# Kernel optimization log

Hardware: AMD Instinct MI355X
Metric: run time of the kernel (lower is better)

The kernel has to match this reference:

```python
import math
import jax, jax.numpy as jnp
import numpy as np

T = 2048       # sequence_length
H = 2048       # hidden_size
NH = 32        # num_attention_heads
NKV = 8        # num_key_value_heads
HD = 64        # head_dim
SW = 128       # sliding_window
QM = NH // NKV # q_mult (GQA group size)
ROPE_THETA = 10000.0
EPS = 1e-5


def setup_inputs() -> dict:
    key = jax.random.key(0)
    k_x, k_s, k_qkv, k_out = jax.random.split(key, 4)
    x = jax.random.normal(k_x, (T, H), dtype=jnp.float32)
    scale = jnp.ones((H,), dtype=jnp.float32)
    sinks = jax.random.normal(k_s, (NH,), dtype=jnp.float32) * 0.02
    qkv_dim = HD * (NH + 2 * NKV)  # 3072
    qkv_kernel = jax.random.normal(k_qkv, (H, qkv_dim), dtype=jnp.float32) * (1.0 / math.sqrt(H))
    qkv_bias = jnp.zeros((qkv_dim,), dtype=jnp.float32)
    out_kernel = jax.random.normal(k_out, (H, H), dtype=jnp.float32) * (1.0 / math.sqrt(H))
    out_bias = jnp.zeros((H,), dtype=jnp.float32)
    # RoPE tables: [T, HD//2]
    half = HD // 2
    inv_freq = 1.0 / (ROPE_THETA ** (np.arange(half, dtype=np.float64) / half))
    ang = np.outer(np.arange(T, dtype=np.float64), inv_freq)
    cos_table = jnp.asarray(np.cos(ang), dtype=jnp.float32)
    sin_table = jnp.asarray(np.sin(ang), dtype=jnp.float32)
    # causal + sliding-window additive mask [T, T]
    qp = np.arange(T, dtype=np.int32)[:, None]
    kp = np.arange(T, dtype=np.int32)[None, :]
    m = np.where(kp > qp, -np.inf, 0.0) + np.where(qp - kp > SW, -np.inf, 0.0)
    mask = jnp.asarray(m, dtype=jnp.float32)
    return dict(x=x, scale=scale, sinks=sinks, qkv_kernel=qkv_kernel,
                qkv_bias=qkv_bias, out_kernel=out_kernel, out_bias=out_bias,
                cos_table=cos_table, sin_table=sin_table, mask=mask)


def _rmsnorm(x, scale):
    t = x.astype(jnp.float32)
    rms = jnp.sqrt(jnp.mean(t * t, axis=-1, keepdims=True) + EPS)
    return ((t / rms) * scale).astype(x.dtype)


def _rope(x, cos, sin):
    # x: [T, ..., HD]; split-half rotation as in the reference RotaryEmbedding
    shp = x.shape
    xr = x.reshape(shp[0], -1, HD)
    c = cos[:, None, :].astype(xr.dtype)
    s = sin[:, None, :].astype(xr.dtype)
    x1, x2 = jnp.split(xr, 2, axis=-1)
    y = jnp.concatenate([x1 * c - x2 * s, x2 * c + x1 * s], axis=-1)
    return y.reshape(shp)


def reference(x, scale, sinks, qkv_kernel, qkv_bias, out_kernel, out_bias,
              cos_table, sin_table, mask):
    normed = _rmsnorm(x, scale)
    qkv = normed @ qkv_kernel + qkv_bias                 # [T, 3072]
    q_end = NH * HD
    k_end = q_end + NKV * HD
    q = qkv[:, :q_end].reshape(T, NKV, QM, HD)           # [T, nkv, qm, hd]
    k = qkv[:, q_end:k_end].reshape(T, NKV, HD)          # [T, nkv, hd]
    v = qkv[:, k_end:].reshape(T, NKV, HD)               # [T, nkv, hd]
    q = _rope(q, cos_table, sin_table)
    k = _rope(k, cos_table, sin_table)
    sm_scale = 1.0 / math.sqrt(float(HD))
    # GQA attention without materializing repeated K/V
    logits = jnp.einsum('qnmd,knd->nmqk', q, k) * sm_scale  # [nkv, qm, T, T]
    logits = logits + mask[None, None, :, :]
    sink_col = jnp.broadcast_to(sinks.reshape(NKV, QM, 1, 1), (NKV, QM, T, 1))
    logits = jnp.concatenate([logits, sink_col], axis=-1)   # [nkv, qm, T, T+1]
    weights = jax.nn.softmax(logits, axis=-1)[..., :-1]     # drop sink column
    attn = jnp.einsum('nmqk,knd->qnmd', weights, v).reshape(T, NH * HD)
    projected = attn @ out_kernel + out_bias
    return x + projected
```

## Files before the change

kernel.cpp:

```cpp
#include <hip/hip_runtime.h>
#include <hip/hip_bf16.h>
#include <stdint.h>

typedef __bf16 bf16_t;
typedef __attribute__((ext_vector_type(8))) __bf16 bf16x8;
typedef __attribute__((ext_vector_type(4))) __bf16 bf16x4;
typedef __attribute__((ext_vector_type(4))) float f32x4;

static constexpr int T_SEQ = 2048;
static constexpr int HID   = 2048;
static constexpr int NHEAD = 32;
static constexpr int NKVH  = 8;
static constexpr int HDIM  = 64;
static constexpr int QKVD  = 3072;

__device__ inline f32x4 mfma16(bf16x8 a, bf16x8 b, f32x4 c) {
    return __builtin_amdgcn_mfma_f32_16x16x32_bf16(a, b, c, 0, 0, 0);
}

__device__ inline void load_lds16(const bf16_t* g, bf16_t* l) {
    __builtin_amdgcn_global_load_lds(
        (const __attribute__((address_space(1))) void*)g,
        (__attribute__((address_space(3))) void*)l, 16, 0, 0);
}

__global__ __launch_bounds__(256) void prep_kernel(const float* __restrict__ Wq,
                                                   const float* __restrict__ Wo,
                                                   bf16_t* __restrict__ Tq,
                                                   bf16_t* __restrict__ To,
                                                   const float* __restrict__ x,
                                                   const float* __restrict__ scale,
                                                   bf16_t* __restrict__ normed) {
    __shared__ float tile[64 * 65];
    int b = blockIdx.x;
    const int t = threadIdx.x;
    if (b < 2560) {
        const float* in; bf16_t* outw; int NN, KK, bx, by;
        if (b < 1536) { in = Wq; outw = Tq; NN = QKVD; KK = HID; bx = b % 48; by = b / 48; }
        else { b -= 1536; in = Wo; outw = To; NN = HID; KK = HID; bx = b % 32; by = b / 32; }
        const int c4 = (t & 15) * 4;
#pragma unroll
        for (int i = 0; i < 4; ++i) {
            int r = (t >> 4) + i * 16;
            float4 v = *(const float4*)(in + (size_t)(by*64 + r) * NN + bx*64 + c4);
            tile[r*65 + c4 + 0] = v.x; tile[r*65 + c4 + 1] = v.y;
            tile[r*65 + c4 + 2] = v.z; tile[r*65 + c4 + 3] = v.w;
        }
        __syncthreads();
        const int kc = t & 7;
#pragma unroll
        for (int i = 0; i < 2; ++i) {
            int n = (t >> 3) + i * 32;
            bf16x8 o;
#pragma unroll
            for (int j = 0; j < 8; ++j) o[j] = (bf16_t)tile[(kc*8 + j)*65 + n];
            *(bf16x8*)(outw + (size_t)(bx*64 + n) * KK + by*64 + kc*8) = o;
        }
    } else {
        int row = b - 2560;
        const float4* x4 = (const float4*)(x + (size_t)row * HID);
        const float4* s4 = (const float4*)scale;
        float4 v0 = x4[t], v1 = x4[t + 256];
        float ss = v0.x*v0.x + v0.y*v0.y + v0.z*v0.z + v0.w*v0.w
                 + v1.x*v1.x + v1.y*v1.y + v1.z*v1.z + v1.w*v1.w;
#pragma unroll
        for (int off = 32; off > 0; off >>= 1) ss += __shfl_down(ss, off);
        if ((t & 63) == 0) tile[t >> 6] = ss;
        __syncthreads();
        float total = tile[0] + tile[1] + tile[2] + tile[3];
        float inv = rsqrtf(total * (1.0f / HID) + 1e-5f);
        float4 sc0 = s4[t], sc1 = s4[t + 256];
        bf16_t* outr = normed + (size_t)row * HID;
        bf16x4 o0, o1;
        o0.x = (bf16_t)(v0.x*inv*sc0.x); o0.y = (bf16_t)(v0.y*inv*sc0.y);
        o0.z = (bf16_t)(v0.z*inv*sc0.z); o0.w = (bf16_t)(v0.w*inv*sc0.w);
        o1.x = (bf16_t)(v1.x*inv*sc1.x); o1.y = (bf16_t)(v1.y*inv*sc1.y);
        o1.z = (bf16_t)(v1.z*inv*sc1.z); o1.w = (bf16_t)(v1.w*inv*sc1.w);
        *(bf16x4*)(outr + 4*t)        = o0;
        *(bf16x4*)(outr + 1024 + 4*t) = o1;
    }
}

__global__ __launch_bounds__(256) void gemm_splitk(const bf16_t* __restrict__ A,
                                                   const bf16_t* __restrict__ Bt,
                                                   bf16_t* __restrict__ Cpart,
                                                   int M, int N, int K) {
    __shared__ __align__(16) bf16_t Asm[3 * 128 * 32];
    __shared__ __align__(16) bf16_t Bsm[3 * 128 * 32];
    const int tid = threadIdx.x;
    const int bm = blockIdx.y * 128, bn = blockIdx.x * 128;
    const int kh = K >> 1;
    const int kb = blockIdx.z * kh;
    const int lane = tid & 63, wave = tid >> 6;
    const int wm = (wave & 1) * 64, wn = (wave >> 1) * 64;
    const int lm = lane & 15, quad = lane >> 4;

    f32x4 acc[4][4];
#pragma unroll
    for (int i = 0; i < 4; ++i)
#pragma unroll
        for (int j = 0; j < 4; ++j) acc[i][j] = (f32x4){0.f, 0.f, 0.f, 0.f};

    const int cid0 = tid, cid1 = tid + 256;
    const int r0 = cid0 >> 2, c0 = (cid0 & 3) ^ ((r0 >> 1) & 3);
    const int r1 = cid1 >> 2, c1 = (cid1 & 3) ^ ((r1 >> 1) & 3);
    const bf16_t* Ab = A  + (size_t)bm * K + kb;
    const bf16_t* Bb = Bt + (size_t)bn * K + kb;
    const size_t ga0 = (size_t)r0 * K + c0 * 8;
    const size_t ga1 = (size_t)r1 * K + c1 * 8;
    const int swz = (quad ^ ((lm >> 1) & 3)) * 8;
    const int ldso = wave * 512;

    const int nsteps = kh >> 5;

#define STAGE(buf, k0) do {                               \
        bf16_t* la_ = &Asm[(buf) * 4096];                 \
        bf16_t* lb_ = &Bsm[(buf) * 4096];                 \
        load_lds16(Ab + ga0 + (k0), la_ + ldso);          \
        load_lds16(Ab + ga1 + (k0), la_ + 2048 + ldso);   \
        load_lds16(Bb + ga0 + (k0), lb_ + ldso);          \
        load_lds16(Bb + ga1 + (k0), lb_ + 2048 + ldso);   \
    } while (0)

    STAGE(0, 0);
    STAGE(1, 32);

    int cur = 0, nxt = 2;
    for (int t = 0; t < nsteps; ++t) {
        if (t + 1 < nsteps) asm volatile("s_waitcnt vmcnt(4)" ::: "memory");
        else                asm volatile("s_waitcnt vmcnt(0)" ::: "memory");
        __builtin_amdgcn_s_barrier();
        __builtin_amdgcn_sched_barrier(0);
        if (t + 2 < nsteps) STAGE(nxt, (t + 2) * 32);

        const bf16_t* __restrict__ Abase = &Asm[cur * 4096];
        const bf16_t* __restrict__ Bbase = &Bsm[cur * 4096];
        bf16x8 af[4], bfr[4];
#pragma unroll
        for (int i = 0; i < 4; ++i)
            af[i]  = *(const bf16x8*)&Abase[(wm + i*16 + lm)*32 + swz];
#pragma unroll
        for (int j = 0; j < 4; ++j)
            bfr[j] = *(const bf16x8*)&Bbase[(wn + j*16 + lm)*32 + swz];
#pragma unroll
        for (int i = 0; i < 4; ++i)
#pragma unroll
            for (int j = 0; j < 4; ++j) acc[i][j] = mfma16(af[i], bfr[j], acc[i][j]);

        cur = (cur == 2) ? 0 : cur + 1;
        nxt = (nxt == 2) ? 0 : nxt + 1;
    }
#undef STAGE

    bf16_t* Cp = Cpart + (size_t)blockIdx.z * M * N;
#pragma unroll
    for (int i = 0; i < 4; ++i) {
        int gr = bm + wm + i*16 + quad*4;
#pragma unroll
        for (int j = 0; j < 4; ++j) {
            int gc = bn + wn + j*16 + lm;
#pragma unroll
            for (int r = 0; r < 4; ++r)
                Cp[(size_t)(gr + r)*N + gc] = (bf16_t)acc[i][j][r];
        }
    }
}

__global__ __launch_bounds__(192) void rope_split(const bf16_t* __restrict__ qp0,
                                                  const bf16_t* __restrict__ qp1,
                                                  const float* __restrict__ qbias,
                                                  const float* __restrict__ cost,
                                                  const float* __restrict__ sint,
                                                  bf16_t* __restrict__ Qb,
                                                  bf16_t* __restrict__ Kb,
                                                  bf16_t* __restrict__ Vb) {
    const int t = blockIdx.x;
    const int hr = threadIdx.x >> 2, p0 = (threadIdx.x & 3) * 8;
    const bf16_t* r0 = qp0 + (size_t)t * QKVD + hr * 64;
    const bf16_t* r1 = qp1 + (size_t)t * QKVD + hr * 64;
    bf16x8 a1 = *(const bf16x8*)(r0 + p0);
    bf16x8 a2 = *(const bf16x8*)(r0 + p0 + 32);
    bf16x8 b1 = *(const bf16x8*)(r1 + p0);
    bf16x8 b2 = *(const bf16x8*)(r1 + p0 + 32);
    const float* qb = qbias + hr * 64;
    float x1[8], x2[8];
#pragma unroll
    for (int j = 0; j < 8; ++j) {
        x1[j] = (float)a1[j] + (float)b1[j] + qb[p0 + j];
        x2[j] = (float)a2[j] + (float)b2[j] + qb[p0 + j + 32];
    }
    bf16x8 w1, w2;
    if (hr < 40) {
        const float* c = cost + (size_t)t * 32 + p0;
        const float* s = sint + (size_t)t * 32 + p0;
#pragma unroll
        for (int j = 0; j < 8; ++j) {
            float cc = c[j], ss = s[j];
            w1[j] = (bf16_t)(x1[j]*cc - x2[j]*ss);
            w2[j] = (bf16_t)(x2[j]*cc + x1[j]*ss);
        }
    } else {
#pragma unroll
        for (int j = 0; j < 8; ++j) { w1[j] = (bf16_t)x1[j]; w2[j] = (bf16_t)x2[j]; }
    }
    bf16_t* dst;
    if (hr < 32)      dst = Qb + ((size_t)t*NHEAD + hr)      * HDIM;
    else if (hr < 40) dst = Kb + ((size_t)t*NKVH + (hr-32))  * HDIM;
    else              dst = Vb + ((size_t)t*NKVH + (hr-40))  * HDIM;
    *(bf16x8*)(dst + p0)      = w1;
    *(bf16x8*)(dst + p0 + 32) = w2;
}

__global__ __launch_bounds__(256) void combine_out(const bf16_t* __restrict__ p0,
                                                   const bf16_t* __restrict__ p1,
                                                   const float* __restrict__ bias,
                                                   const float* __restrict__ x,
                                                   float* __restrict__ out) {
    const int n4 = T_SEQ * HID / 4;
    for (int i4 = blockIdx.x * 256 + threadIdx.x; i4 < n4; i4 += gridDim.x * 256) {
        bf16x4 a = *(const bf16x4*)(p0 + (size_t)i4 * 4);
        bf16x4 b = *(const bf16x4*)(p1 + (size_t)i4 * 4);
        float4 xv = *(const float4*)(x + (size_t)i4 * 4);
        int col4 = (i4 * 4) & (HID - 1);
        float4 bi = *(const float4*)(bias + col4);
        float4 o;
        o.x = (float)a.x + (float)b.x + bi.x + xv.x;
        o.y = (float)a.y + (float)b.y + bi.y + xv.y;
        o.z = (float)a.z + (float)b.z + bi.z + xv.z;
        o.w = (float)a.w + (float)b.w + bi.w + xv.w;
        *(float4*)(out + (size_t)i4 * 4) = o;
    }
}

__global__ __launch_bounds__(256) void attn_kernel(const bf16_t* __restrict__ Qb,
                                                   const bf16_t* __restrict__ Kb,
                                                   const bf16_t* __restrict__ Vb,
                                                   const float* __restrict__ sinks,
                                                   bf16_t* __restrict__ attnb) {
    __shared__ __align__(16) bf16_t Vt[64 * 200];
    __shared__ __align__(16) bf16_t Ws[64 * 200];

    const int tid = threadIdx.x;
    const int qt = blockIdx.x, h = blockIdx.y;
    const int qs = qt * 64;
    const int nkv = h >> 2;

    {
        const int off = (tid >> 5) * 8;
#pragma unroll
        for (int it = 0; it < 3; ++it) {
            int j2 = (tid & 31) + 32 * it;
            int kg0 = qs - 128 + 2*j2;     if (kg0 < 0) kg0 = 0;
            int kg1 = qs - 128 + 2*j2 + 1; if (kg1 < 0) kg1 = 0;
            union { uint4 u; bf16_t e[8]; } v0, v1;
            v0.u = *(const uint4*)(Vb + ((size_t)kg0*NKVH + nkv)*HDIM + off);
            v1.u = *(const uint4*)(Vb + ((size_t)kg1*NKVH + nkv)*HDIM + off);
#pragma unroll
            for (int r = 0; r < 8; ++r) {
                union { uint u; bf16_t e[2]; } p;
                p.e[0] = v0.e[r]; p.e[1] = v1.e[r];
                *(uint*)&Vt[(off + r)*200 + 2*j2] = p.u;
            }
        }
    }

    const int lane = tid & 63, wave = tid >> 6;
    const int lm = lane & 15, quad = lane >> 4;
    const int w16 = wave * 16;

    f32x4 S[12];
#pragma unroll
    for (int jt = 0; jt < 12; ++jt) S[jt] = (f32x4){0.f, 0.f, 0.f, 0.f};
    const bf16_t* Qrow = Qb + ((size_t)(qs + w16 + lm)*NHEAD + h)*HDIM + quad*8;
    int krow[12];
#pragma unroll
    for (int jt = 0; jt < 12; ++jt) {
        int kg = qs - 128 + jt*16 + lm;
        krow[jt] = kg < 0 ? 0 : kg;
    }
#pragma unroll
    for (int ks = 0; ks < 2; ++ks) {
        bf16x8 aq = *(const bf16x8*)(Qrow + ks*32);
#pragma unroll
        for (int jt = 0; jt < 12; ++jt) {
            bf16x8 bk = *(const bf16x8*)(Kb + ((size_t)krow[jt]*NKVH + nkv)*HDIM + ks*32 + quad*8);
            S[jt] = mfma16(aq, bk, S[jt]);
        }
    }

    const float sink = sinks[h];
#pragma unroll
    for (int reg = 0; reg < 4; ++reg) {
        const int qg = qs + w16 + quad*4 + reg;
        float mx = -1e30f;
#pragma unroll
        for (int jt = 0; jt < 12; ++jt) {
            int kg = qs - 128 + jt*16 + lm;
            float sv = S[jt][reg] * 0.125f;
            bool valid = (kg >= 0) && (kg <= qg) && (qg - kg <= 128);
            sv = valid ? sv : -1e30f;
            S[jt][reg] = sv;
            mx = fmaxf(mx, sv);
        }
#pragma unroll
        for (int off = 1; off < 16; off <<= 1) mx = fmaxf(mx, __shfl_xor(mx, off));
        float M = fmaxf(mx, sink);
        float sum = 0.f;
#pragma unroll
        for (int jt = 0; jt < 12; ++jt) {
            float e = __expf(S[jt][reg] - M);
            S[jt][reg] = e; sum += e;
        }
#pragma unroll
        for (int off = 1; off < 16; off <<= 1) sum += __shfl_xor(sum, off);
        float rden = 1.f / (sum + __expf(sink - M));
#pragma unroll
        for (int jt = 0; jt < 12; ++jt)
            Ws[(w16 + quad*4 + reg)*200 + jt*16 + lm] = (bf16_t)(S[jt][reg] * rden);
    }
    __syncthreads();

    f32x4 O[4];
#pragma unroll
    for (int nt = 0; nt < 4; ++nt) O[nt] = (f32x4){0.f, 0.f, 0.f, 0.f};
#pragma unroll
    for (int ks = 0; ks < 6; ++ks) {
        bf16x8 aw = *(const bf16x8*)&Ws[(w16 + lm)*200 + ks*32 + quad*8];
#pragma unroll
        for (int nt = 0; nt < 4; ++nt) {
            bf16x8 bv = *(const bf16x8*)&Vt[(nt*16 + lm)*200 + ks*32 + quad*8];
            O[nt] = mfma16(aw, bv, O[nt]);
        }
    }
#pragma unroll
    for (int nt = 0; nt < 4; ++nt)
#pragma unroll
        for (int reg = 0; reg < 4; ++reg)
            attnb[(size_t)(qs + w16 + quad*4 + reg)*HID + h*HDIM + nt*16 + lm] =
                (bf16_t)(O[nt][reg]);
}

extern "C" void kernel_launch(void* const* d_in, const int* in_sizes, int n_in,
                              void* d_out, int out_size, void* d_ws, size_t ws_size,
                              hipStream_t stream) {
    (void)in_sizes; (void)n_in; (void)out_size; (void)ws_size;
    const float* x          = (const float*)d_in[0];
    const float* scale      = (const float*)d_in[1];
    const float* sinks      = (const float*)d_in[2];
    const float* qkv_kernel = (const float*)d_in[3];
    const float* qkv_bias   = (const float*)d_in[4];
    const float* out_kernel = (const float*)d_in[5];
    const float* out_bias   = (const float*)d_in[6];
    const float* cos_t      = (const float*)d_in[7];
    const float* sin_t      = (const float*)d_in[8];
    float* out = (float*)d_out;

    char* ws = (char*)d_ws;
    const size_t MiB = 1048576;
    bf16_t* Wt_out = (bf16_t*)(ws);
    bf16_t* Wt_qkv = (bf16_t*)(ws + 8*MiB);
    bf16_t* attnb  = (bf16_t*)(ws + 8*MiB);
    bf16_t* normed = (bf16_t*)(ws + 20*MiB);
    bf16_t* qkvp   = (bf16_t*)(ws + 28*MiB);
    bf16_t* outp   = (bf16_t*)(ws + 28*MiB);
    bf16_t* Qb     = (bf16_t*)(ws + 52*MiB);
    bf16_t* Kb     = (bf16_t*)(ws + 60*MiB);
    bf16_t* Vb     = (bf16_t*)(ws + 62*MiB);

    prep_kernel<<<4608, 256, 0, stream>>>(qkv_kernel, out_kernel, Wt_qkv, Wt_out,
                                          x, scale, normed);
    gemm_splitk<<<dim3(QKVD/128, T_SEQ/128, 2), 256, 0, stream>>>(normed, Wt_qkv, qkvp,
                                                                  T_SEQ, QKVD, HID);
    rope_split<<<T_SEQ, 192, 0, stream>>>(qkvp, qkvp + (size_t)T_SEQ*QKVD, qkv_bias,
                                          cos_t, sin_t, Qb, Kb, Vb);
    attn_kernel<<<dim3(T_SEQ/64, NHEAD), 256, 0, stream>>>(Qb, Kb, Vb, sinks, attnb);
    gemm_splitk<<<dim3(HID/128, T_SEQ/128, 2), 256, 0, stream>>>(attnb, Wt_out, outp,
                                                                 T_SEQ, HID, HID);
    combine_out<<<2048, 256, 0, stream>>>(outp, outp + (size_t)T_SEQ*HID, out_bias, x, out);
}
```

Before: 224.6 us.

## Fuse RoPE/split-K reduction into attention and process a KV group per block

```diff
diff --git a/kernel.cpp b/kernel.cpp
--- a/kernel.cpp
+++ b/kernel.cpp
@@ -164,51 +164,6 @@
                 Cp[(size_t)(gr + r)*N + gc] = (bf16_t)acc[i][j][r];
         }
     }
-}
-
-__global__ __launch_bounds__(192) void rope_split(const bf16_t* __restrict__ qp0,
-                                                  const bf16_t* __restrict__ qp1,
-                                                  const float* __restrict__ qbias,
-                                                  const float* __restrict__ cost,
-                                                  const float* __restrict__ sint,
-                                                  bf16_t* __restrict__ Qb,
-                                                  bf16_t* __restrict__ Kb,
-                                                  bf16_t* __restrict__ Vb) {
-    const int t = blockIdx.x;
-    const int hr = threadIdx.x >> 2, p0 = (threadIdx.x & 3) * 8;
-    const bf16_t* r0 = qp0 + (size_t)t * QKVD + hr * 64;
-    const bf16_t* r1 = qp1 + (size_t)t * QKVD + hr * 64;
-    bf16x8 a1 = *(const bf16x8*)(r0 + p0);
-    bf16x8 a2 = *(const bf16x8*)(r0 + p0 + 32);
-    bf16x8 b1 = *(const bf16x8*)(r1 + p0);
-    bf16x8 b2 = *(const bf16x8*)(r1 + p0 + 32);
-    const float* qb = qbias + hr * 64;
-    float x1[8], x2[8];
-#pragma unroll
-    for (int j = 0; j < 8; ++j) {
-        x1[j] = (float)a1[j] + (float)b1[j] + qb[p0 + j];
-        x2[j] = (float)a2[j] + (float)b2[j] + qb[p0 + j + 32];
-    }
-    bf16x8 w1, w2;
-    if (hr < 40) {
-        const float* c = cost + (size_t)t * 32 + p0;
-        const float* s = sint + (size_t)t * 32 + p0;
-#pragma unroll
-        for (int j = 0; j < 8; ++j) {
-            float cc = c[j], ss = s[j];
-            w1[j] = (bf16_t)(x1[j]*cc - x2[j]*ss);
-            w2[j] = (bf16_t)(x2[j]*cc + x1[j]*ss);
-        }
-    } else {
-#pragma unroll
-        for (int j = 0; j < 8; ++j) { w1[j] = (bf16_t)x1[j]; w2[j] = (bf16_t)x2[j]; }
-    }
-    bf16_t* dst;
-    if (hr < 32)      dst = Qb + ((size_t)t*NHEAD + hr)      * HDIM;
-    else if (hr < 40) dst = Kb + ((size_t)t*NKVH + (hr-32))  * HDIM;
-    else              dst = Vb + ((size_t)t*NKVH + (hr-40))  * HDIM;
-    *(bf16x8*)(dst + p0)      = w1;
-    *(bf16x8*)(dst + p0 + 32) = w2;
 }
 
 __global__ __launch_bounds__(256) void combine_out(const bf16_t* __restrict__ p0,
@@ -232,112 +187,165 @@
     }
 }
 
-__global__ __launch_bounds__(256) void attn_kernel(const bf16_t* __restrict__ Qb,
-                                                   const bf16_t* __restrict__ Kb,
-                                                   const bf16_t* __restrict__ Vb,
-                                                   const float* __restrict__ sinks,
-                                                   bf16_t* __restrict__ attnb) {
+__global__ __launch_bounds__(512, 2) void attn_fused(const bf16_t* __restrict__ qp0,
+                                                     const bf16_t* __restrict__ qp1,
+                                                     const float* __restrict__ qkvb,
+                                                     const float* __restrict__ cost,
+                                                     const float* __restrict__ sint,
+                                                     const float* __restrict__ sinks,
+                                                     bf16_t* __restrict__ attnb) {
     __shared__ __align__(16) bf16_t Vt[64 * 200];
-    __shared__ __align__(16) bf16_t Ws[64 * 200];
+    __shared__ __align__(16) bf16_t Ws[128 * 200];
 
     const int tid = threadIdx.x;
-    const int qt = blockIdx.x, h = blockIdx.y;
+    const int qt = blockIdx.x, nkv = blockIdx.y;
     const int qs = qt * 64;
-    const int nkv = h >> 2;
 
     {
-        const int off = (tid >> 5) * 8;
-#pragma unroll
-        for (int it = 0; it < 3; ++it) {
-            int j2 = (tid & 31) + 32 * it;
-            int kg0 = qs - 128 + 2*j2;     if (kg0 < 0) kg0 = 0;
-            int kg1 = qs - 128 + 2*j2 + 1; if (kg1 < 0) kg1 = 0;
-            union { uint4 u; bf16_t e[8]; } v0, v1;
-            v0.u = *(const uint4*)(Vb + ((size_t)kg0*NKVH + nkv)*HDIM + off);
-            v1.u = *(const uint4*)(Vb + ((size_t)kg1*NKVH + nkv)*HDIM + off);
-#pragma unroll
-            for (int r = 0; r < 8; ++r) {
-                union { uint u; bf16_t e[2]; } p;
-                p.e[0] = v0.e[r]; p.e[1] = v1.e[r];
-                *(uint*)&Vt[(off + r)*200 + 2*j2] = p.u;
+        const int off = (tid >> 6) * 8;
+        const int j2l = tid & 63;
+        const float* vb = qkvb + 2560 + nkv * 64;
+#pragma unroll
+        for (int it = 0; it < 2; ++it) {
+            int j2 = j2l + 64 * it;
+            if (j2 < 96) {
+                int kg0 = qs - 128 + 2 * j2;     if (kg0 < 0) kg0 = 0;
+                int kg1 = qs - 128 + 2 * j2 + 1; if (kg1 < 0) kg1 = 0;
+                const size_t o0 = (size_t)kg0 * QKVD + 2560 + nkv * 64 + off;
+                const size_t o1 = (size_t)kg1 * QKVD + 2560 + nkv * 64 + off;
+                bf16x8 a0 = *(const bf16x8*)(qp0 + o0), b0 = *(const bf16x8*)(qp1 + o0);
+                bf16x8 a1 = *(const bf16x8*)(qp0 + o1), b1 = *(const bf16x8*)(qp1 + o1);
+#pragma unroll
+                for (int r = 0; r < 8; ++r) {
+                    union { uint u; bf16_t e[2]; } p;
+                    p.e[0] = (bf16_t)((float)a0[r] + (float)b0[r] + vb[off + r]);
+                    p.e[1] = (bf16_t)((float)a1[r] + (float)b1[r] + vb[off + r]);
+                    *(uint*)&Vt[(off + r) * 200 + 2 * j2] = p.u;
+                }
             }
         }
     }
 
     const int lane = tid & 63, wave = tid >> 6;
     const int lm = lane & 15, quad = lane >> 4;
-    const int w16 = wave * 16;
-
-    f32x4 S[12];
-#pragma unroll
-    for (int jt = 0; jt < 12; ++jt) S[jt] = (f32x4){0.f, 0.f, 0.f, 0.f};
-    const bf16_t* Qrow = Qb + ((size_t)(qs + w16 + lm)*NHEAD + h)*HDIM + quad*8;
+    const int r16 = (wave & 3) * 16;
+    const int hp  = (wave >> 2) * 2;
+
     int krow[12];
 #pragma unroll
     for (int jt = 0; jt < 12; ++jt) {
-        int kg = qs - 128 + jt*16 + lm;
+        int kg = qs - 128 + jt * 16 + lm;
         krow[jt] = kg < 0 ? 0 : kg;
     }
-#pragma unroll
-    for (int ks = 0; ks < 2; ++ks) {
-        bf16x8 aq = *(const bf16x8*)(Qrow + ks*32);
+    bf16x8 kf0[12], kf1[12];
+    {
+        const float* kb = qkvb + 2048 + nkv * 64;
 #pragma unroll
         for (int jt = 0; jt < 12; ++jt) {
-            bf16x8 bk = *(const bf16x8*)(Kb + ((size_t)krow[jt]*NKVH + nkv)*HDIM + ks*32 + quad*8);
-            S[jt] = mfma16(aq, bk, S[jt]);
-        }
-    }
-
-    const float sink = sinks[h];
-#pragma unroll
-    for (int reg = 0; reg < 4; ++reg) {
-        const int qg = qs + w16 + quad*4 + reg;
-        float mx = -1e30f;
-#pragma unroll
-        for (int jt = 0; jt < 12; ++jt) {
-            int kg = qs - 128 + jt*16 + lm;
-            float sv = S[jt][reg] * 0.125f;
-            bool valid = (kg >= 0) && (kg <= qg) && (qg - kg <= 128);
-            sv = valid ? sv : -1e30f;
-            S[jt][reg] = sv;
-            mx = fmaxf(mx, sv);
-        }
-#pragma unroll
-        for (int off = 1; off < 16; off <<= 1) mx = fmaxf(mx, __shfl_xor(mx, off));
-        float M = fmaxf(mx, sink);
-        float sum = 0.f;
-#pragma unroll
-        for (int jt = 0; jt < 12; ++jt) {
-            float e = __expf(S[jt][reg] - M);
-            S[jt][reg] = e; sum += e;
-        }
-#pragma unroll
-        for (int off = 1; off < 16; off <<= 1) sum += __shfl_xor(sum, off);
-        float rden = 1.f / (sum + __expf(sink - M));
-#pragma unroll
-        for (int jt = 0; jt < 12; ++jt)
-            Ws[(w16 + quad*4 + reg)*200 + jt*16 + lm] = (bf16_t)(S[jt][reg] * rden);
-    }
+            const size_t ko = (size_t)krow[jt] * QKVD + 2048 + nkv * 64 + quad * 8;
+            bf16x8 a0 = *(const bf16x8*)(qp0 + ko);
+            bf16x8 a1 = *(const bf16x8*)(qp0 + ko + 32);
+            bf16x8 b0 = *(const bf16x8*)(qp1 + ko);
+            bf16x8 b1 = *(const bf16x8*)(qp1 + ko + 32);
+            const float* c = cost + (size_t)krow[jt] * 32 + quad * 8;
+            const float* s = sint + (size_t)krow[jt] * 32 + quad * 8;
+#pragma unroll
+            for (int j = 0; j < 8; ++j) {
+                float x1 = (float)a0[j] + (float)b0[j] + kb[quad * 8 + j];
+                float x2 = (float)a1[j] + (float)b1[j] + kb[quad * 8 + j + 32];
+                float cc = c[j], ssn = s[j];
+                kf0[jt][j] = (bf16_t)(x1 * cc - x2 * ssn);
+                kf1[jt][j] = (bf16_t)(x2 * cc + x1 * ssn);
+            }
+        }
+    }
+
     __syncthreads();
 
-    f32x4 O[4];
-#pragma unroll
-    for (int nt = 0; nt < 4; ++nt) O[nt] = (f32x4){0.f, 0.f, 0.f, 0.f};
-#pragma unroll
-    for (int ks = 0; ks < 6; ++ks) {
-        bf16x8 aw = *(const bf16x8*)&Ws[(w16 + lm)*200 + ks*32 + quad*8];
-#pragma unroll
-        for (int nt = 0; nt < 4; ++nt) {
-            bf16x8 bv = *(const bf16x8*)&Vt[(nt*16 + lm)*200 + ks*32 + quad*8];
-            O[nt] = mfma16(aw, bv, O[nt]);
-        }
-    }
-#pragma unroll
-    for (int nt = 0; nt < 4; ++nt)
-#pragma unroll
-        for (int reg = 0; reg < 4; ++reg)
-            attnb[(size_t)(qs + w16 + quad*4 + reg)*HID + h*HDIM + nt*16 + lm] =
-                (bf16_t)(O[nt][reg]);
+#pragma unroll
+    for (int h2p = 0; h2p < 2; ++h2p) {
+        const int h = nkv * 4 + hp + h2p;
+
+        bf16x8 aq0, aq1;
+        {
+            const int qrow = qs + r16 + lm;
+            const size_t qo = (size_t)qrow * QKVD + h * 64 + quad * 8;
+            bf16x8 a0 = *(const bf16x8*)(qp0 + qo);
+            bf16x8 a1 = *(const bf16x8*)(qp0 + qo + 32);
+            bf16x8 b0 = *(const bf16x8*)(qp1 + qo);
+            bf16x8 b1 = *(const bf16x8*)(qp1 + qo + 32);
+            const float* qb = qkvb + h * 64;
+            const float* c = cost + (size_t)qrow * 32 + quad * 8;
+            const float* s = sint + (size_t)qrow * 32 + quad * 8;
+#pragma unroll
+            for (int j = 0; j < 8; ++j) {
+                float x1 = (float)a0[j] + (float)b0[j] + qb[quad * 8 + j];
+                float x2 = (float)a1[j] + (float)b1[j] + qb[quad * 8 + j + 32];
+                float cc = c[j], ssn = s[j];
+                aq0[j] = (bf16_t)(x1 * cc - x2 * ssn);
+                aq1[j] = (bf16_t)(x2 * cc + x1 * ssn);
+            }
+        }
+
+        f32x4 S[12];
+#pragma unroll
+        for (int jt = 0; jt < 12; ++jt) S[jt] = (f32x4){0.f, 0.f, 0.f, 0.f};
+#pragma unroll
+        for (int jt = 0; jt < 12; ++jt) S[jt] = mfma16(aq0, kf0[jt], S[jt]);
+#pragma unroll
+        for (int jt = 0; jt < 12; ++jt) S[jt] = mfma16(aq1, kf1[jt], S[jt]);
+
+        const float sink = sinks[h];
+#pragma unroll
+        for (int reg = 0; reg < 4; ++reg) {
+            const int qg = qs + r16 + quad * 4 + reg;
+            float mx = -1e30f;
+#pragma unroll
+            for (int jt = 0; jt < 12; ++jt) {
+                int kg = qs - 128 + jt * 16 + lm;
+                float sv = S[jt][reg] * 0.125f;
+                bool valid = (kg >= 0) && (kg <= qg) && (qg - kg <= 128);
+                sv = valid ? sv : -1e30f;
+                S[jt][reg] = sv;
+                mx = fmaxf(mx, sv);
+            }
+#pragma unroll
+            for (int off = 1; off < 16; off <<= 1) mx = fmaxf(mx, __shfl_xor(mx, off));
+            float M = fmaxf(mx, sink);
+            float sum = 0.f;
+#pragma unroll
+            for (int jt = 0; jt < 12; ++jt) {
+                float e = __expf(S[jt][reg] - M);
+                S[jt][reg] = e; sum += e;
+            }
+#pragma unroll
+            for (int off = 1; off < 16; off <<= 1) sum += __shfl_xor(sum, off);
+            float rden = 1.f / (sum + __expf(sink - M));
+#pragma unroll
+            for (int jt = 0; jt < 12; ++jt)
+                Ws[(wave * 16 + quad * 4 + reg) * 200 + jt * 16 + lm] =
+                    (bf16_t)(S[jt][reg] * rden);
+        }
+
+        f32x4 O[4];
+#pragma unroll
+        for (int nt = 0; nt < 4; ++nt) O[nt] = (f32x4){0.f, 0.f, 0.f, 0.f};
+#pragma unroll
+        for (int ks = 0; ks < 6; ++ks) {
+            bf16x8 aw = *(const bf16x8*)&Ws[(wave * 16 + lm) * 200 + ks * 32 + quad * 8];
+#pragma unroll
+            for (int nt = 0; nt < 4; ++nt) {
+                bf16x8 bv = *(const bf16x8*)&Vt[(nt * 16 + lm) * 200 + ks * 32 + quad * 8];
+                O[nt] = mfma16(aw, bv, O[nt]);
+            }
+        }
+#pragma unroll
+        for (int nt = 0; nt < 4; ++nt)
+#pragma unroll
+            for (int reg = 0; reg < 4; ++reg)
+                attnb[(size_t)(qs + r16 + quad * 4 + reg) * HID + h * HDIM + nt * 16 + lm] =
+                    (bf16_t)(O[nt][reg]);
+    }
 }
 
 extern "C" void kernel_launch(void* const* d_in, const int* in_sizes, int n_in,
@@ -363,17 +371,14 @@
     bf16_t* normed = (bf16_t*)(ws + 20*MiB);
     bf16_t* qkvp   = (bf16_t*)(ws + 28*MiB);
     bf16_t* outp   = (bf16_t*)(ws + 28*MiB);
-    bf16_t* Qb     = (bf16_t*)(ws + 52*MiB);
-    bf16_t* Kb     = (bf16_t*)(ws + 60*MiB);
-    bf16_t* Vb     = (bf16_t*)(ws + 62*MiB);
 
     prep_kernel<<<4608, 256, 0, stream>>>(qkv_kernel, out_kernel, Wt_qkv, Wt_out,
                                           x, scale, normed);
     gemm_splitk<<<dim3(QKVD/128, T_SEQ/128, 2), 256, 0, stream>>>(normed, Wt_qkv, qkvp,
                                                                   T_SEQ, QKVD, HID);
-    rope_split<<<T_SEQ, 192, 0, stream>>>(qkvp, qkvp + (size_t)T_SEQ*QKVD, qkv_bias,
-                                          cos_t, sin_t, Qb, Kb, Vb);
-    attn_kernel<<<dim3(T_SEQ/64, NHEAD), 256, 0, stream>>>(Qb, Kb, Vb, sinks, attnb);
+    attn_fused<<<dim3(T_SEQ/64, NKVH), 512, 0, stream>>>(qkvp, qkvp + (size_t)T_SEQ*QKVD,
+                                                         qkv_bias, cos_t, sin_t, sinks,
+                                                         attnb);
     gemm_splitk<<<dim3(HID/128, T_SEQ/128, 2), 256, 0, stream>>>(attnb, Wt_out, outp,
                                                                  T_SEQ, HID, HID);
     combine_out<<<2048, 256, 0, stream>>>(outp, outp + (size_t)T_SEQ*HID, out_bias, x, out);
```

After: 229.1 us. About the same (+2.0%).
